# Performance work log

Hardware: AMD Instinct MI355X
Metric: run time of the kernel (lower is better)

Reference implementation:

```python
import jax, jax.numpy as jnp
import numpy as np

B, H, W, C, L, E, HID = 16, 128, 128, 64, 8, 8, 4
LEVELS = [4, 4, 4, 4, 4, 4, 4, 4]
SQ2 = 0.7071067811865476  # 1/sqrt(2), orthonormal Haar


def conv1x1(x, w, b):
    # x: (B,Ci,H,W), w: (Co,Ci) -> (B,Co,H,W)
    return jnp.einsum('bixy,oi->boxy', x, w) + b[None, :, None, None]


def mish(t):
    return t * jnp.tanh(jax.nn.softplus(t))


def dwt2(x):
    # one level of separable orthonormal Haar DWT (stand-in for the DTCWT filters)
    lo = (x[..., ::2, :] + x[..., 1::2, :]) * SQ2
    hi = (x[..., ::2, :] - x[..., 1::2, :]) * SQ2
    ll = (lo[..., ::2] + lo[..., 1::2]) * SQ2
    lh = (lo[..., ::2] - lo[..., 1::2]) * SQ2
    hl = (hi[..., ::2] + hi[..., 1::2]) * SQ2
    hh = (hi[..., ::2] - hi[..., 1::2]) * SQ2
    return ll, lh, hl, hh


def _ileave_cols(a, b):
    out = jnp.stack([a, b], axis=-1)
    return out.reshape(a.shape[:-1] + (a.shape[-1] * 2,))


def _ileave_rows(a, b):
    out = jnp.stack([a, b], axis=-2)  # (...,h,2,w)
    return out.reshape(a.shape[:-2] + (a.shape[-2] * 2, a.shape[-1]))


def idwt2(ll, lh, hl, hh):
    lo = _ileave_cols((ll + lh) * SQ2, (ll - lh) * SQ2)
    hi = _ileave_cols((hl + hh) * SQ2, (hl - hh) * SQ2)
    return _ileave_rows((lo + hi) * SQ2, (lo - hi) * SQ2)


def wave_conv(x, w, level):
    # WaveConv2dcwt: multi-level decomposition, channel-mix coarsest approx +
    # coarsest detail bands via (Ci,Co) kernels, then reconstruct.
    det = []
    a = x
    for _ in range(level):
        a, lh, hl, hh = dwt2(a)
        det.append((lh, hl, hh))
    mix = lambda t, m: jnp.einsum('bixy,io->boxy', t, m)
    a = mix(a, w[0])
    lh, hl, hh = det[-1]
    det[-1] = (mix(lh, w[1]), mix(hl, w[2]), mix(hh, w[3]))
    for lh, hl, hh in reversed(det):
        a = idwt2(a, lh, hl, hh)
    return a


def setup_inputs() -> dict:
    key = jax.random.key(0)
    ks = jax.random.split(key, 16)
    p = lambda k, sh, s=0.08: (jax.random.normal(k, sh, jnp.float32) * s)
    return {
        'x': jax.random.normal(ks[0], (B, 1, H, W), jnp.float32),
        'label': jax.random.normal(ks[1], (L,), jnp.float32),
        'fc0_w': p(ks[2], (C, 3), 0.3), 'fc0_b': p(ks[3], (C,), 0.02),
        'fc1_w': p(ks[4], (C, C)), 'fc1_b': p(ks[5], (C,), 0.02),
        'gate_Wg': p(ks[6], (HID, L, E), 0.3), 'gate_vg': p(ks[7], (HID, E), 0.3),
        'exp_w': p(ks[8], (HID, 8, 4, C, C)),
        'w0_w': p(ks[9], (HID, C, C)), 'w0_b': p(ks[10], (HID, C), 0.02),
        'fc2_w': p(ks[11], (128, C)), 'fc2_b': p(ks[12], (128,), 0.02),
        'fc3_w': p(ks[13], (1, 128)), 'fc3_b': p(ks[14], (1,), 0.02),
    }


def reference(x, label, fc0_w, fc0_b, fc1_w, fc1_b, gate_Wg, gate_vg, exp_w,
              w0_w, w0_b, fc2_w, fc2_b, fc3_w, fc3_b):
    b, _, h_, w_ = x.shape
    gx = jnp.linspace(0.0, 1.0, h_, dtype=jnp.float32).reshape(1, 1, h_, 1)
    gy = jnp.linspace(0.0, 1.0, w_, dtype=jnp.float32).reshape(1, 1, 1, w_)
    grid = jnp.concatenate([jnp.broadcast_to(gx, (b, 1, h_, w_)),
                            jnp.broadcast_to(gy, (b, 1, h_, w_))], axis=1)
    h = conv1x1(jnp.concatenate([x, grid], axis=1), fc0_w, fc0_b)
    h = conv1x1(h, fc1_w, fc1_b)
    # gates: all hidden-layer lambdas computed from the post-fc1 activations
    lab = jnp.broadcast_to(label[None, None, :], (b, C, L))
    pooled = jnp.mean(h, axis=(2, 3))  # (B,C)
    logits = jnp.einsum('bcl,hle->hbce', lab, gate_Wg) \
        + pooled[None, :, :, None] * gate_vg[:, None, None, :]
    lams = jax.nn.softmax(logits, axis=-1)  # (HID,B,C,E)
    for hd in range(HID):
        lam = lams[hd]
        # original forward reuses experts 4,5 for lambda slots 6,7 -> fold weights
        wts = jnp.stack([lam[..., 0], lam[..., 1], lam[..., 2], lam[..., 3],
                         lam[..., 4] + lam[..., 6], lam[..., 5] + lam[..., 7]],
                        axis=-1)  # (B,C,6)
        y = jnp.zeros_like(h)
        for e in range(6):
            y = y + wts[..., e][:, :, None, None] * wave_conv(h, exp_w[hd, e], LEVELS[e])
        h = y + conv1x1(h, w0_w[hd], w0_b[hd])
        if hd != HID - 1:
            h = mish(h)
    h = mish(conv1x1(h, fc2_w, fc2_b))
    return conv1x1(h, fc3_w, fc3_b)
```

## Files before the change

kernel.cpp:

```cpp
#include <hip/hip_runtime.h>
#include <math.h>

#define Bn 16
#define Cn 64
#define NPIX 16384
#define HIDN 4

typedef unsigned short ushort_t;
typedef short bf16x8 __attribute__((ext_vector_type(8)));
typedef float f32x4 __attribute__((ext_vector_type(4)));
#define MFMA16 __builtin_amdgcn_mfma_f32_16x16x32_bf16

#define WS_H     0
#define WS_W2B   16777216
#define WS_G0    (WS_W2B + 256)
#define WS_XM    (WS_G0 + 32)
#define WS_WTS   (WS_XM + 16)
#define WS_AP    (WS_WTS + 24576)
#define WS_BANDS (WS_AP + 262144)
#define WS_CORR  (WS_BANDS + 262144)
#define WS_FC2S  (WS_CORR + 262144)
#define WS_W0S   (WS_FC2S + 8192)

__device__ __forceinline__ float mishf(float t) {
    float a = 1.0f + expf(fminf(t, 40.0f));
    a = a * a;
    return t * (a - 1.0f) / (a + 1.0f);
}

__device__ __forceinline__ void split_bf16(float x, ushort_t& hi, ushort_t& lo) {
    unsigned u = __float_as_uint(x);
    unsigned r = (u + 0x7FFFu + ((u >> 16) & 1u)) >> 16;
    hi = (ushort_t)r;
    float l = x - __uint_as_float(r << 16);
    lo = (ushort_t)(__float_as_uint(l) >> 16);
}

__global__ void prep_kernel(const float* __restrict__ fc0_w, const float* __restrict__ fc0_b,
                            const float* __restrict__ fc1_w, const float* __restrict__ fc1_b,
                            const float* __restrict__ label, const float* __restrict__ Wg,
                            float* __restrict__ ws) {
    int t = threadIdx.x;
    if (t < 64) {
        int c = t;
        float a0 = 0.f, a1 = 0.f, a2 = 0.f, ab = 0.f;
        for (int k = 0; k < 64; ++k) {
            float f = fc1_w[c * 64 + k];
            a0 += f * fc0_w[k * 3 + 0];
            a1 += f * fc0_w[k * 3 + 1];
            a2 += f * fc0_w[k * 3 + 2];
            ab += f * fc0_b[k];
        }
        ws[WS_W2B + c * 4 + 0] = a0;
        ws[WS_W2B + c * 4 + 1] = a1;
        ws[WS_W2B + c * 4 + 2] = a2;
        ws[WS_W2B + c * 4 + 3] = ab + fc1_b[c];
    } else if (t < 96) {
        int idx = t - 64;
        int hd = idx >> 3, e = idx & 7;
        float s = 0.f;
        for (int l = 0; l < 8; ++l) s += label[l] * Wg[(hd * 8 + l) * 8 + e];
        ws[WS_G0 + idx] = s;
    }
}

__global__ void wsplit_kernel(const float* __restrict__ w0_w, const float* __restrict__ fc2_w,
                              float* __restrict__ ws) {
    int gid = blockIdx.x * 256 + threadIdx.x;
    ushort_t* w0hi = (ushort_t*)(ws + WS_W0S);
    ushort_t* w0lo = w0hi + 16384;
    ushort_t* fc2hi = (ushort_t*)(ws + WS_FC2S);
    ushort_t* fc2lo = fc2hi + 8192;
    if (gid < 16384) {
        int o = (gid >> 6) & 63, i = gid & 63;
        float v = w0_w[gid] + ((o == i) ? 1.0f : 0.0f);
        ushort_t h, l; split_bf16(v, h, l);
        w0hi[gid] = h; w0lo[gid] = l;
    } else if (gid < 24576) {
        int k = gid - 16384;
        ushort_t h, l; split_bf16(fc2_w[k], h, l);
        fc2hi[k] = h; fc2lo[k] = l;
    }
}

__global__ void xmean_kernel(const float* __restrict__ x, float* __restrict__ ws) {
    int b = blockIdx.x, t = threadIdx.x;
    float s = 0.f;
    for (int i = t; i < NPIX; i += 256) s += x[b * NPIX + i];
    for (int off = 32; off > 0; off >>= 1) s += __shfl_down(s, off);
    __shared__ float ps[4];
    if ((t & 63) == 0) ps[t >> 6] = s;
    __syncthreads();
    if (t == 0) ws[WS_XM + b] = (ps[0] + ps[1] + ps[2] + ps[3]) * (1.0f / NPIX);
}

__global__ void gates_kernel(const float* __restrict__ vg, float* __restrict__ ws) {
    int b = blockIdx.x, t = threadIdx.x;
    int c = t & 63, hd = t >> 6;
    const float* W2 = ws + WS_W2B + c * 4;
    float pooled = W2[0] * ws[WS_XM + b] + 0.5f * (W2[1] + W2[2]) + W2[3];
    float lg[8], m = -1e30f;
    for (int e = 0; e < 8; ++e) {
        lg[e] = ws[WS_G0 + hd * 8 + e] + pooled * vg[hd * 8 + e];
        m = fmaxf(m, lg[e]);
    }
    float s = 0.f;
    for (int e = 0; e < 8; ++e) { lg[e] = expf(lg[e] - m); s += lg[e]; }
    float inv = 1.0f / s;
    float* o = ws + WS_WTS + ((hd * 16 + b) * 64 + c) * 6;
    o[0] = lg[0] * inv; o[1] = lg[1] * inv; o[2] = lg[2] * inv;
    o[3] = lg[3] * inv; o[4] = (lg[4] + lg[6]) * inv; o[5] = (lg[5] + lg[7]) * inv;
}

__global__ void h1_kernel(const float* __restrict__ x, float* __restrict__ ws) {
    int gid = blockIdx.x * 256 + threadIdx.x;
    int base = gid * 4;
    int b = base >> 20;
    int rem = base & 1048575;
    int c = rem >> 14;
    int pix = rem & 16383;
    int p = pix >> 7, q = pix & 127;
    const float* W2 = ws + WS_W2B + c * 4;
    float w0 = W2[0], w1 = W2[1], w2 = W2[2], bb = W2[3];
    float4 xv = *(const float4*)(x + b * NPIX + pix);
    float gx = p * (1.0f / 127.0f);
    float gy0 = q * (1.0f / 127.0f);
    const float step = 1.0f / 127.0f;
    float4 o;
    o.x = w0 * xv.x + w1 * gx + w2 * gy0 + bb;
    o.y = w0 * xv.y + w1 * gx + w2 * (gy0 + step) + bb;
    o.z = w0 * xv.z + w1 * gx + w2 * (gy0 + 2.f * step) + bb;
    o.w = w0 * xv.w + w1 * gx + w2 * (gy0 + 3.f * step) + bb;
    *(float4*)(ws + WS_H + base) = o;
}

__global__ void ap_kernel(const float* __restrict__ exp_w, float* __restrict__ ws, int hd) {
    int flat = blockIdx.x * 256 + threadIdx.x;
    int o = flat & 63;
    int i = (flat >> 6) & 63;
    int k = (flat >> 12) & 3;
    int b = flat >> 14;
    float acc = (i == o) ? -1.0f : 0.0f;
    const float* w = ws + WS_WTS + ((hd * 16 + b) * 64 + o) * 6;
    const float* ew = exp_w + (size_t)((hd * 8) * 4 + k) * 4096 + i * 64 + o;
    #pragma unroll
    for (int e = 0; e < 6; ++e) acc += w[e] * ew[(size_t)e * 16384];
    ws[WS_AP + flat] = acc;
}

__global__ void bands_kernel(const float* __restrict__ hbuf, float* __restrict__ ws) {
    int bi = blockIdx.x;
    int b = bi >> 6, c = bi & 63;
    int t = threadIdx.x;
    __shared__ float R[128][17];
    __shared__ float S[16][17];
    const float* plane = hbuf + (size_t)(b * 64 + c) * NPIX;
    for (int rb = 0; rb < 8; ++rb) {
        const float* p4 = plane + rb * 2048 + t * 8;
        float4 a = *(const float4*)p4;
        float4 bb = *(const float4*)(p4 + 4);
        R[rb * 16 + (t >> 4)][t & 15] = a.x + a.y + a.z + a.w + bb.x + bb.y + bb.z + bb.w;
    }
    __syncthreads();
    {
        int rb2 = t >> 4, g = t & 15;
        float s = 0.f;
        #pragma unroll
        for (int k = 0; k < 8; ++k) s += R[rb2 * 8 + k][g];
        S[rb2][g] = s;
    }
    __syncthreads();
    if (t < 64) {
        int X = t >> 3, Y = t & 7;
        float q00 = S[2 * X][2 * Y],     q01 = S[2 * X][2 * Y + 1];
        float q10 = S[2 * X + 1][2 * Y], q11 = S[2 * X + 1][2 * Y + 1];
        float* bd = ws + WS_BANDS + (size_t)b * 16384 + c * 64 + t;
        bd[0]     = (q00 + q01 + q10 + q11) * 0.0625f;
        bd[4096]  = (q00 - q01 + q10 - q11) * 0.0625f;
        bd[8192]  = (q00 + q01 - q10 - q11) * 0.0625f;
        bd[12288] = (q00 - q01 - q10 + q11) * 0.0625f;
    }
}

__global__ void mix_kernel(float* __restrict__ ws) {
    int bi = blockIdx.x;
    int t = threadIdx.x;
    __shared__ float sA[64][65];
    __shared__ float sB[64][64];
    const float* Ap = ws + WS_AP + (size_t)bi * 4096;
    const float* Bd = ws + WS_BANDS + (size_t)bi * 4096;
    for (int it = 0; it < 16; ++it) {
        int flat = it * 256 + t;
        sA[flat >> 6][flat & 63] = Ap[flat];
        sB[flat >> 6][flat & 63] = Bd[flat];
    }
    __syncthreads();
    int xy = t & 63, ob = (t >> 6) * 16;
    float acc[16];
    #pragma unroll
    for (int j = 0; j < 16; ++j) acc[j] = 0.f;
    for (int i = 0; i < 64; ++i) {
        float v = sB[i][xy];
        #pragma unroll
        for (int j = 0; j < 16; ++j) acc[j] = fmaf(sA[i][ob + j], v, acc[j]);
    }
    float* out = ws + WS_CORR + (size_t)bi * 4096 + xy;
    #pragma unroll
    for (int j = 0; j < 16; ++j) out[(ob + j) * 64] = acc[j];
}

__global__ void __launch_bounds__(256) conv_mfma(
        float* __restrict__ hbuf, const float* __restrict__ ws,
        const float* __restrict__ w0_b, int hd, int act) {
    int bi = blockIdx.x;
    int b = bi >> 8, r = bi & 255;
    int row = r >> 1, qh = (r & 1) * 64;
    int t = threadIdx.x;
    __shared__ short sBhi[64][72];
    __shared__ short sBlo[64][72];
    __shared__ float sCorr[8][64];

    const float* hbase = hbuf + (size_t)b * 64 * NPIX + row * 128 + qh;
    {
        int px = t & 63, lane4 = t >> 6;
        for (int rep = 0; rep < 8; ++rep) {
            int c0 = rep * 8 + lane4 * 2;
            float v0 = hbase[(size_t)c0 * NPIX + px];
            float v1 = hbase[(size_t)(c0 + 1) * NPIX + px];
            ushort_t h0, l0, h1, l1;
            split_bf16(v0, h0, l0);
            split_bf16(v1, h1, l1);
            *(unsigned*)&sBhi[px][c0] = (unsigned)h0 | ((unsigned)h1 << 16);
            *(unsigned*)&sBlo[px][c0] = (unsigned)l0 | ((unsigned)l1 << 16);
        }
    }
    {
        int X = row >> 4;
        float si = ((row >> 3) & 1) ? -1.f : 1.f;
        for (int rep = 0; rep < 2; ++rep) {
            int idx = rep * 256 + t;
            int o = idx & 63, qg = idx >> 6;
            int Y = (r & 1) * 4 + (qg >> 1);
            float sj = (qg & 1) ? -1.f : 1.f;
            const float* cb = ws + WS_CORR + (size_t)b * 16384 + o * 64 + X * 8 + Y;
            sCorr[qg][o] = w0_b[hd * 64 + o] +
                           0.0625f * (cb[0] + sj * cb[4096] + si * cb[8192] + si * sj * cb[12288]);
        }
    }
    int w = t >> 6, l = t & 63;
    int lr = l & 15, lk = l >> 4;
    const ushort_t* w0hi = (const ushort_t*)(ws + WS_W0S) + hd * 4096;
    const ushort_t* w0lo = w0hi + 16384;
    bf16x8 Ah[4][2], Al[4][2];
    #pragma unroll
    for (int m = 0; m < 4; ++m) {
        int o0 = 16 * m + lr;
        Ah[m][0] = *(const bf16x8*)(w0hi + o0 * 64 + 8 * lk);
        Ah[m][1] = *(const bf16x8*)(w0hi + o0 * 64 + 32 + 8 * lk);
        Al[m][0] = *(const bf16x8*)(w0lo + o0 * 64 + 8 * lk);
        Al[m][1] = *(const bf16x8*)(w0lo + o0 * 64 + 32 + 8 * lk);
    }
    __syncthreads();

    int px = 16 * w + lr;
    bf16x8 Bh0 = *(const bf16x8*)&sBhi[px][8 * lk];
    bf16x8 Bh1 = *(const bf16x8*)&sBhi[px][32 + 8 * lk];
    bf16x8 Bl0 = *(const bf16x8*)&sBlo[px][8 * lk];
    bf16x8 Bl1 = *(const bf16x8*)&sBlo[px][32 + 8 * lk];
    int qg = px >> 3;
    float* outp = hbuf + (size_t)(b * 64 + 4 * lk) * NPIX + row * 128 + qh + px;
    #pragma unroll
    for (int m = 0; m < 4; ++m) {
        f32x4 a = {0.f, 0.f, 0.f, 0.f};
        a = MFMA16(Ah[m][0], Bh0, a, 0, 0, 0);
        a = MFMA16(Ah[m][1], Bh1, a, 0, 0, 0);
        a = MFMA16(Ah[m][0], Bl0, a, 0, 0, 0);
        a = MFMA16(Ah[m][1], Bl1, a, 0, 0, 0);
        a = MFMA16(Al[m][0], Bh0, a, 0, 0, 0);
        a = MFMA16(Al[m][1], Bh1, a, 0, 0, 0);
        float4 c4 = *(const float4*)&sCorr[qg][16 * m + 4 * lk];
        float cv[4] = {c4.x, c4.y, c4.z, c4.w};
        #pragma unroll
        for (int rr = 0; rr < 4; ++rr) {
            float v = a[rr] + cv[rr];
            if (act) v = mishf(v);
            outp[(size_t)(16 * m + rr) * NPIX] = v;
        }
    }
}

__global__ void __launch_bounds__(256) final_mfma(
        const float* __restrict__ hbuf, const float* __restrict__ ws,
        const float* __restrict__ fc2_b, const float* __restrict__ fc3_w,
        const float* __restrict__ fc3_b, float* __restrict__ out) {
    int bi = blockIdx.x;
    int b = bi >> 8, r = bi & 255;
    int row = r >> 1, qh = (r & 1) * 64;
    int t = threadIdx.x;
    __shared__ short sBhi[64][72];
    __shared__ short sBlo[64][72];
    __shared__ float sB2[128];
    __shared__ float sF3[128];

    const float* hbase = hbuf + (size_t)b * 64 * NPIX + row * 128 + qh;
    {
        int px = t & 63, lane4 = t >> 6;
        for (int rep = 0; rep < 8; ++rep) {
            int c0 = rep * 8 + lane4 * 2;
            float v0 = hbase[(size_t)c0 * NPIX + px];
            float v1 = hbase[(size_t)(c0 + 1) * NPIX + px];
            ushort_t h0, l0, h1, l1;
            split_bf16(v0, h0, l0);
            split_bf16(v1, h1, l1);
            *(unsigned*)&sBhi[px][c0] = (unsigned)h0 | ((unsigned)h1 << 16);
            *(unsigned*)&sBlo[px][c0] = (unsigned)l0 | ((unsigned)l1 << 16);
        }
        if (t < 128) { sB2[t] = fc2_b[t]; sF3[t] = fc3_w[t]; }
    }
    __syncthreads();

    int w = t >> 6, l = t & 63;
    int lr = l & 15, lk = l >> 4;
    int px = 16 * w + lr;
    const ushort_t* fc2hi = (const ushort_t*)(ws + WS_FC2S);
    const ushort_t* fc2lo = fc2hi + 8192;
    bf16x8 Bh0 = *(const bf16x8*)&sBhi[px][8 * lk];
    bf16x8 Bh1 = *(const bf16x8*)&sBhi[px][32 + 8 * lk];
    bf16x8 Bl0 = *(const bf16x8*)&sBlo[px][8 * lk];
    bf16x8 Bl1 = *(const bf16x8*)&sBlo[px][32 + 8 * lk];
    float partial = 0.f;
    #pragma unroll
    for (int m = 0; m < 8; ++m) {
        int j0 = 16 * m + lr;
        bf16x8 Ah0 = *(const bf16x8*)(fc2hi + j0 * 64 + 8 * lk);
        bf16x8 Ah1 = *(const bf16x8*)(fc2hi + j0 * 64 + 32 + 8 * lk);
        bf16x8 Al0 = *(const bf16x8*)(fc2lo + j0 * 64 + 8 * lk);
        bf16x8 Al1 = *(const bf16x8*)(fc2lo + j0 * 64 + 32 + 8 * lk);
        f32x4 a = {0.f, 0.f, 0.f, 0.f};
        a = MFMA16(Ah0, Bh0, a, 0, 0, 0);
        a = MFMA16(Ah1, Bh1, a, 0, 0, 0);
        a = MFMA16(Ah0, Bl0, a, 0, 0, 0);
        a = MFMA16(Ah1, Bl1, a, 0, 0, 0);
        a = MFMA16(Al0, Bh0, a, 0, 0, 0);
        a = MFMA16(Al1, Bh1, a, 0, 0, 0);
        float4 b4 = *(const float4*)&sB2[16 * m + 4 * lk];
        float4 f4 = *(const float4*)&sF3[16 * m + 4 * lk];
        float bv[4] = {b4.x, b4.y, b4.z, b4.w};
        float fv[4] = {f4.x, f4.y, f4.z, f4.w};
        #pragma unroll
        for (int rr = 0; rr < 4; ++rr)
            partial = fmaf(fv[rr], mishf(a[rr] + bv[rr]), partial);
    }
    partial += __shfl_xor(partial, 16, 64);
    partial += __shfl_xor(partial, 32, 64);
    if (lk == 0)
        out[(size_t)b * NPIX + row * 128 + qh + px] = partial + fc3_b[0];
}

extern "C" void kernel_launch(void* const* d_in, const int* in_sizes, int n_in,
                              void* d_out, int out_size, void* d_ws, size_t ws_size,
                              hipStream_t stream) {
    const float* x      = (const float*)d_in[0];
    const float* label  = (const float*)d_in[1];
    const float* fc0_w  = (const float*)d_in[2];
    const float* fc0_b  = (const float*)d_in[3];
    const float* fc1_w  = (const float*)d_in[4];
    const float* fc1_b  = (const float*)d_in[5];
    const float* gate_Wg = (const float*)d_in[6];
    const float* gate_vg = (const float*)d_in[7];
    const float* exp_w  = (const float*)d_in[8];
    const float* w0_w   = (const float*)d_in[9];
    const float* w0_b   = (const float*)d_in[10];
    const float* fc2_w  = (const float*)d_in[11];
    const float* fc2_b  = (const float*)d_in[12];
    const float* fc3_w  = (const float*)d_in[13];
    const float* fc3_b  = (const float*)d_in[14];
    float* out = (float*)d_out;
    float* ws = (float*)d_ws;
    float* hbuf = ws + WS_H;

    prep_kernel<<<1, 256, 0, stream>>>(fc0_w, fc0_b, fc1_w, fc1_b, label, gate_Wg, ws);
    wsplit_kernel<<<96, 256, 0, stream>>>(w0_w, fc2_w, ws);
    xmean_kernel<<<16, 256, 0, stream>>>(x, ws);
    gates_kernel<<<16, 256, 0, stream>>>(gate_vg, ws);
    h1_kernel<<<16384, 256, 0, stream>>>(x, ws);
    for (int hd = 0; hd < HIDN; ++hd) {
        ap_kernel<<<1024, 256, 0, stream>>>(exp_w, ws, hd);
        bands_kernel<<<1024, 256, 0, stream>>>(hbuf, ws);
        mix_kernel<<<64, 256, 0, stream>>>(ws);
        conv_mfma<<<4096, 256, 0, stream>>>(hbuf, ws, w0_b, hd, hd != HIDN - 1);
    }
    final_mfma<<<4096, 256, 0, stream>>>(hbuf, ws, fc2_b, fc3_w, fc3_b, out);
}
```

Before: 505.1 us.

## Fuse 8x8 block-sum pooling into producer kernels via atomics, drop bands pass

Replaces the separate bands_kernel, which re-read the full 64MB activation buffer on every hidden layer, with per-8x8-block partial sums accumulated by atomics in the h1 and conv_mfma epilogues. A small kernel then turns those sums into the four Haar bands. The mish function also moves to fast __expf/__fdividef intrinsics. This adds atomic traffic, shuffles and zeroing launches, and makes the sums order-nondeterministic.

Result: slower. 574.6 us (+13.7%).

```diff
diff --git a/kernel.cpp b/kernel.cpp
--- a/kernel.cpp
+++ b/kernel.cpp
@@ -21,11 +21,13 @@
 #define WS_CORR  (WS_BANDS + 262144)
 #define WS_FC2S  (WS_CORR + 262144)
 #define WS_W0S   (WS_FC2S + 8192)
+#define WS_QS    (WS_W0S + 16384)
 
 __device__ __forceinline__ float mishf(float t) {
-    float a = 1.0f + expf(fminf(t, 40.0f));
-    a = a * a;
-    return t * (a - 1.0f) / (a + 1.0f);
+    float e = __expf(fminf(t, 30.0f));
+    float a = 1.0f + e;
+    float a2 = a * a;
+    return t * __fdividef(a2 - 1.0f, a2 + 1.0f);
 }
 
 __device__ __forceinline__ void split_bf16(float x, ushort_t& hi, ushort_t& lo) {
@@ -81,6 +83,25 @@
         ushort_t h, l; split_bf16(fc2_w[k], h, l);
         fc2hi[k] = h; fc2lo[k] = l;
     }
+}
+
+__global__ void qszero_kernel(float* __restrict__ ws) {
+    int gid = blockIdx.x * 256 + threadIdx.x;
+    *(float4*)(ws + WS_QS + gid * 4) = make_float4(0.f, 0.f, 0.f, 0.f);
+}
+
+__global__ void qs2bands_kernel(float* __restrict__ ws) {
+    int flat = blockIdx.x * 256 + threadIdx.x;
+    int b = flat >> 12, c = (flat >> 6) & 63, cell = flat & 63;
+    int X = cell >> 3, Y = cell & 7;
+    const float* Q = ws + WS_QS + ((b * 64 + c) << 8);
+    float q00 = Q[(2 * X) * 16 + 2 * Y],     q01 = Q[(2 * X) * 16 + 2 * Y + 1];
+    float q10 = Q[(2 * X + 1) * 16 + 2 * Y], q11 = Q[(2 * X + 1) * 16 + 2 * Y + 1];
+    float* bd = ws + WS_BANDS + (size_t)b * 16384 + c * 64 + cell;
+    bd[0]     = (q00 + q01 + q10 + q11) * 0.0625f;
+    bd[4096]  = (q00 - q01 + q10 - q11) * 0.0625f;
+    bd[8192]  = (q00 + q01 - q10 - q11) * 0.0625f;
+    bd[12288] = (q00 - q01 - q10 + q11) * 0.0625f;
 }
 
 __global__ void xmean_kernel(const float* __restrict__ x, float* __restrict__ ws) {
@@ -132,6 +153,10 @@
     o.z = w0 * xv.z + w1 * gx + w2 * (gy0 + 2.f * step) + bb;
     o.w = w0 * xv.w + w1 * gx + w2 * (gy0 + 3.f * step) + bb;
     *(float4*)(ws + WS_H + base) = o;
+    float s = o.x + o.y + o.z + o.w;
+    s += __shfl_xor(s, 1);
+    if (!(threadIdx.x & 1))
+        atomicAdd(ws + WS_QS + ((b * 64 + c) * 16 + (p >> 3)) * 16 + (q >> 3), s);
 }
 
 __global__ void ap_kernel(const float* __restrict__ exp_w, float* __restrict__ ws, int hd) {
@@ -146,40 +171,6 @@
     #pragma unroll
     for (int e = 0; e < 6; ++e) acc += w[e] * ew[(size_t)e * 16384];
     ws[WS_AP + flat] = acc;
-}
-
-__global__ void bands_kernel(const float* __restrict__ hbuf, float* __restrict__ ws) {
-    int bi = blockIdx.x;
-    int b = bi >> 6, c = bi & 63;
-    int t = threadIdx.x;
-    __shared__ float R[128][17];
-    __shared__ float S[16][17];
-    const float* plane = hbuf + (size_t)(b * 64 + c) * NPIX;
-    for (int rb = 0; rb < 8; ++rb) {
-        const float* p4 = plane + rb * 2048 + t * 8;
-        float4 a = *(const float4*)p4;
-        float4 bb = *(const float4*)(p4 + 4);
-        R[rb * 16 + (t >> 4)][t & 15] = a.x + a.y + a.z + a.w + bb.x + bb.y + bb.z + bb.w;
-    }
-    __syncthreads();
-    {
-        int rb2 = t >> 4, g = t & 15;
-        float s = 0.f;
-        #pragma unroll
-        for (int k = 0; k < 8; ++k) s += R[rb2 * 8 + k][g];
-        S[rb2][g] = s;
-    }
-    __syncthreads();
-    if (t < 64) {
-        int X = t >> 3, Y = t & 7;
-        float q00 = S[2 * X][2 * Y],     q01 = S[2 * X][2 * Y + 1];
-        float q10 = S[2 * X + 1][2 * Y], q11 = S[2 * X + 1][2 * Y + 1];
-        float* bd = ws + WS_BANDS + (size_t)b * 16384 + c * 64 + t;
-        bd[0]     = (q00 + q01 + q10 + q11) * 0.0625f;
-        bd[4096]  = (q00 - q01 + q10 - q11) * 0.0625f;
-        bd[8192]  = (q00 + q01 - q10 - q11) * 0.0625f;
-        bd[12288] = (q00 - q01 - q10 + q11) * 0.0625f;
-    }
 }
 
 __global__ void mix_kernel(float* __restrict__ ws) {
@@ -210,7 +201,7 @@
 }
 
 __global__ void __launch_bounds__(256) conv_mfma(
-        float* __restrict__ hbuf, const float* __restrict__ ws,
+        float* __restrict__ hbuf, float* __restrict__ ws,
         const float* __restrict__ w0_b, int hd, int act) {
     int bi = blockIdx.x;
     int b = bi >> 8, r = bi & 255;
@@ -268,6 +259,8 @@
     bf16x8 Bl0 = *(const bf16x8*)&sBlo[px][8 * lk];
     bf16x8 Bl1 = *(const bf16x8*)&sBlo[px][32 + 8 * lk];
     int qg = px >> 3;
+    int X2 = row >> 3, Y2 = (qh + px) >> 3;
+    float* qsb = ws + WS_QS + (size_t)(b * 64) * 256;
     float* outp = hbuf + (size_t)(b * 64 + 4 * lk) * NPIX + row * 128 + qh + px;
     #pragma unroll
     for (int m = 0; m < 4; ++m) {
@@ -285,6 +278,16 @@
             float v = a[rr] + cv[rr];
             if (act) v = mishf(v);
             outp[(size_t)(16 * m + rr) * NPIX] = v;
+            if (act) {
+                float s = v;
+                s += __shfl_xor(s, 1);
+                s += __shfl_xor(s, 2);
+                s += __shfl_xor(s, 4);
+                if ((lr & 7) == 0) {
+                    int o = 16 * m + 4 * lk + rr;
+                    atomicAdd(qsb + (o * 16 + X2) * 16 + Y2, s);
+                }
+            }
         }
     }
 }
@@ -383,11 +386,13 @@
     wsplit_kernel<<<96, 256, 0, stream>>>(w0_w, fc2_w, ws);
     xmean_kernel<<<16, 256, 0, stream>>>(x, ws);
     gates_kernel<<<16, 256, 0, stream>>>(gate_vg, ws);
+    qszero_kernel<<<256, 256, 0, stream>>>(ws);
     h1_kernel<<<16384, 256, 0, stream>>>(x, ws);
     for (int hd = 0; hd < HIDN; ++hd) {
         ap_kernel<<<1024, 256, 0, stream>>>(exp_w, ws, hd);
-        bands_kernel<<<1024, 256, 0, stream>>>(hbuf, ws);
+        qs2bands_kernel<<<256, 256, 0, stream>>>(ws);
         mix_kernel<<<64, 256, 0, stream>>>(ws);
+        qszero_kernel<<<256, 256, 0, stream>>>(ws);
         conv_mfma<<<4096, 256, 0, stream>>>(hbuf, ws, w0_b, hd, hd != HIDN - 1);
     }
     final_mfma<<<4096, 256, 0, stream>>>(hbuf, ws, fc2_b, fc3_w, fc3_b, out);
```
